# Kernel tuning notes

Hardware: AMD Instinct MI355X
Metric: run time of the kernel (lower is better)

## Reference

```python
import jax, jax.numpy as jnp
import numpy as np

N_NODES = 20000
HEADS = 4


def _gat_conv(x, src, dst, W, att_src, att_dst, bias, concat):
    # PyG GATConv: h = x @ W -> [N, H, C]; edge score = leaky_relu(a_s[src]+a_d[dst], 0.2);
    # segment softmax over dst; scatter-add weighted messages.
    N = x.shape[0]
    H, C = att_src.shape[1], att_src.shape[2]
    h = (x @ W).reshape(N, H, C)
    a_s = jnp.sum(h * att_src, axis=-1)  # [N, H]
    a_d = jnp.sum(h * att_dst, axis=-1)  # [N, H]
    e = jax.nn.leaky_relu(a_s[src] + a_d[dst], negative_slope=0.2)  # [E, H]
    m = jax.ops.segment_max(e, dst, num_segments=N)  # [N, H]
    e = jnp.exp(e - m[dst])
    denom = jax.ops.segment_sum(e, dst, num_segments=N)
    alpha = e / (denom[dst] + 1e-16)  # [E, H]
    msg = h[src] * alpha[:, :, None]  # [E, H, C]
    out = jax.ops.segment_sum(msg, dst, num_segments=N)  # [N, H, C]
    if concat:
        out = out.reshape(N, H * C)
    else:
        out = out.mean(axis=1)
    return out + bias


def setup_inputs() -> dict:
    key = jax.random.key(0)
    ks = jax.random.split(key, 16)
    N, F_in, Hd, H, Z = N_NODES, 256, 128, HEADS, 64
    E = 320000
    x = jax.random.normal(ks[0], (N, F_in), dtype=jnp.float32)
    edge_index = jax.random.randint(ks[1], (2, E), 0, N, dtype=jnp.int64)
    def xavier(k, shape):
        fan_in, fan_out = shape[0], shape[1]
        lim = float(np.sqrt(6.0 / (fan_in + fan_out)))
        return jax.random.uniform(k, shape, jnp.float32, -lim, lim)
    inp = {"x": x, "edge_index": edge_index}
    dims = [(F_in, Hd), (Hd * H, Hd), (Hd * H, Hd)]
    for i, (din, dout) in enumerate(dims, 1):
        inp[f"W{i}"] = xavier(ks[2 * i], (din, H * dout))
        inp[f"att{i}_src"] = jax.random.normal(ks[2 * i + 1], (1, H, dout), dtype=jnp.float32) * 0.1
        inp[f"att{i}_dst"] = jax.random.normal(jax.random.fold_in(ks[2 * i + 1], 7), (1, H, dout), dtype=jnp.float32) * 0.1
        bdim = H * dout if i < 3 else dout
        inp[f"b{i}"] = jnp.zeros((bdim,), dtype=jnp.float32)
    inp["fc_W"] = xavier(ks[10], (Hd, 2 * Z))
    inp["fc_b"] = jnp.zeros((2 * Z,), dtype=jnp.float32)
    return inp


def reference(x, edge_index, W1, att1_src, att1_dst, b1, W2, att2_src, att2_dst, b2,
              W3, att3_src, att3_dst, b3, fc_W, fc_b):
    N = x.shape[0]
    # add_self_loops=True (PyG default)
    loop = jnp.arange(N, dtype=edge_index.dtype)
    src = jnp.concatenate([edge_index[0], loop])
    dst = jnp.concatenate([edge_index[1], loop])
    h = jax.nn.leaky_relu(_gat_conv(x, src, dst, W1, att1_src, att1_dst, b1, True), 0.01)
    h = jax.nn.leaky_relu(_gat_conv(h, src, dst, W2, att2_src, att2_dst, b2, True), 0.01)
    h = _gat_conv(h, src, dst, W3, att3_src, att3_dst, b3, False)
    z = h @ fc_W + fc_b
    mu, logvar = jnp.split(z, 2, axis=1)
    return (mu, jnp.exp(logvar))
```

## Files before the change

### kernel.cpp

```cpp
#include <hip/hip_runtime.h>
#include <hip/hip_bf16.h>

typedef unsigned short u16;
typedef unsigned int u32;
typedef __attribute__((ext_vector_type(8))) short bf16x8;
typedef __attribute__((ext_vector_type(4))) float f32x4;
typedef __attribute__((ext_vector_type(8))) u16 u16x8;
typedef __attribute__((ext_vector_type(4))) u16 u16x4;

#define NN 20000
#define NE 320000
#define HC 512

__device__ __forceinline__ float bf2f(u16 u){ return __uint_as_float(((u32)u)<<16); }
__device__ __forceinline__ u16 f2bf(float x){
  __hip_bfloat16 h = __float2bfloat16(x);
  return *reinterpret_cast<u16*>(&h);
}
__device__ __forceinline__ float escore(float x){
  float e = x > 0.f ? x : 0.2f*x;
  return __expf(fminf(e, 80.f));
}

__global__ __launch_bounds__(256) void cast_kernel(const float* __restrict__ in, u16* __restrict__ out, int total){
  int i = (blockIdx.x*256 + threadIdx.x)*4;
  if (i >= total) return;
  float4 v = *(const float4*)(in + i);
  u16x4 o = { f2bf(v.x), f2bf(v.y), f2bf(v.z), f2bf(v.w) };
  *(u16x4*)(out + i) = o;
}

__global__ __launch_bounds__(256) void transpose_cast(const float* __restrict__ W, u16* __restrict__ WT,
                                                      int K, int N){
  __shared__ u16 t[32][33];
  int bx = blockIdx.x*32;
  int by = blockIdx.y*32;
  int tx = threadIdx.x & 31, ty = threadIdx.x >> 5;
  for (int r = ty; r < 32; r += 8) t[r][tx] = f2bf(W[(size_t)(by+r)*N + bx + tx]);
  __syncthreads();
  for (int r = ty; r < 32; r += 8) WT[(size_t)(bx+r)*K + by + tx] = t[tx][r];
}

__global__ void detect_kernel(const int* __restrict__ ei, int* __restrict__ flag){
  __shared__ int nz;
  if (threadIdx.x == 0) nz = 0;
  __syncthreads();
  int c = 0;
  for (int k = threadIdx.x; k < 4096; k += 256) if (ei[2*k + 1] != 0) c++;
  atomicAdd(&nz, c);
  __syncthreads();
  if (threadIdx.x == 0) *flag = (nz == 0) ? 1 : 0;
}

__global__ __launch_bounds__(256) void normalize_edges(const int* __restrict__ ei, const int* __restrict__ flag,
    int* __restrict__ src, int* __restrict__ dst, int E){
  int e = blockIdx.x*256 + threadIdx.x;
  if (e >= E) return;
  if (*flag){ src[e] = ei[2*e]; dst[e] = ei[2*(E + e)]; }
  else      { src[e] = ei[e];   dst[e] = ei[E + e]; }
}

__global__ __launch_bounds__(256) void gemm_bf16(const u16* __restrict__ A, const u16* __restrict__ BT,
                                                 u16* __restrict__ C, int M, int K){
  __shared__ __align__(16) u16 Ads[128][64];
  __shared__ __align__(16) u16 Bds[128][64];
  const int bm = blockIdx.x, bn = blockIdx.y;
  const int tid = threadIdx.x;
  const int lane = tid & 63, wid = tid >> 6;
  const int wr = (wid >> 1) << 6, wc = (wid & 1) << 6;
  f32x4 acc[4][4] = {};
  const int row0 = bm*128;
  for (int k0 = 0; k0 < K; k0 += 64){
    #pragma unroll
    for (int p = 0; p < 4; ++p){
      int idx = p*256 + tid;
      int r = idx >> 3;
      int c = (idx & 7) << 3;
      int cs = c ^ ((r & 7) << 3);
      u16x8 va = {};
      int gr = row0 + r;
      if (gr < M) va = *(const u16x8*)(A + (size_t)gr*K + k0 + c);
      *(u16x8*)&Ads[r][cs] = va;
      u16x8 vb = *(const u16x8*)(BT + (size_t)(bn*128 + r)*K + k0 + c);
      *(u16x8*)&Bds[r][cs] = vb;
    }
    __syncthreads();
    #pragma unroll
    for (int kk = 0; kk < 64; kk += 32){
      const int lr = lane & 15;
      const int lk = kk + ((lane >> 4) << 3);
      bf16x8 a[4], b[4];
      #pragma unroll
      for (int i = 0; i < 4; ++i){
        int ar = wr + 16*i + lr;
        a[i] = *(const bf16x8*)&Ads[ar][lk ^ ((ar & 7) << 3)];
      }
      #pragma unroll
      for (int j = 0; j < 4; ++j){
        int br = wc + 16*j + lr;
        b[j] = *(const bf16x8*)&Bds[br][lk ^ ((br & 7) << 3)];
      }
      #pragma unroll
      for (int i = 0; i < 4; ++i)
        #pragma unroll
        for (int j = 0; j < 4; ++j)
          acc[i][j] = __builtin_amdgcn_mfma_f32_16x16x32_bf16(a[i], b[j], acc[i][j], 0, 0, 0);
    }
    __syncthreads();
  }
  const int lr = lane & 15, r4 = (lane >> 4) << 2;
  #pragma unroll
  for (int i = 0; i < 4; ++i)
    #pragma unroll
    for (int j = 0; j < 4; ++j){
      int col = bn*128 + wc + 16*j + lr;
      #pragma unroll
      for (int r = 0; r < 4; ++r){
        int row = row0 + wr + 16*i + r4 + r;
        if (row < M) C[(size_t)row*HC + col] = f2bf(acc[i][j][r]);
      }
    }
}

__global__ __launch_bounds__(256) void asad_kernel(const u16* __restrict__ h,
    const float* __restrict__ attS, const float* __restrict__ attD,
    float* __restrict__ a_s, float* __restrict__ a_d, int N){
  int wid = blockIdx.x*4 + (threadIdx.x >> 6);
  if (wid >= N) return;
  int lane = threadIdx.x & 63;
  u16x8 v = *(const u16x8*)(h + (size_t)wid*HC + lane*8);
  float4 s0 = *(const float4*)(attS + lane*8);
  float4 s1 = *(const float4*)(attS + lane*8 + 4);
  float4 d0 = *(const float4*)(attD + lane*8);
  float4 d1 = *(const float4*)(attD + lane*8 + 4);
  float sv[8] = {s0.x,s0.y,s0.z,s0.w,s1.x,s1.y,s1.z,s1.w};
  float dv[8] = {d0.x,d0.y,d0.z,d0.w,d1.x,d1.y,d1.z,d1.w};
  float ps = 0.f, pd = 0.f;
  #pragma unroll
  for (int t = 0; t < 8; ++t){ float hv = bf2f(v[t]); ps += hv*sv[t]; pd += hv*dv[t]; }
  #pragma unroll
  for (int off = 1; off < 16; off <<= 1){
    ps += __shfl_xor(ps, off, 64);
    pd += __shfl_xor(pd, off, 64);
  }
  if ((lane & 15) == 0){
    int hh = lane >> 4;
    a_s[wid*4 + hh] = ps;
    a_d[wid*4 + hh] = pd;
  }
}

__global__ __launch_bounds__(256) void hist_kernel(const int* __restrict__ dst, int* __restrict__ cnt, int E){
  int e = blockIdx.x*256 + threadIdx.x;
  if (e < E) atomicAdd(&cnt[dst[e]], 1);
}

__global__ __launch_bounds__(1024) void scan_kernel(const int* __restrict__ cnt,
    int* __restrict__ offs, int* __restrict__ cur, int N){
  __shared__ int bsum[1024];
  int tid = threadIdx.x;
  const int CH = (N + 1023) >> 10;
  int lo = tid*CH, hi = min(lo + CH, N);
  int s = 0;
  for (int i = lo; i < hi; ++i) s += cnt[i];
  bsum[tid] = s;
  __syncthreads();
  for (int off = 1; off < 1024; off <<= 1){
    int t = (tid >= off) ? bsum[tid - off] : 0;
    __syncthreads();
    bsum[tid] += t;
    __syncthreads();
  }
  int run = (tid > 0) ? bsum[tid - 1] : 0;
  for (int i = lo; i < hi; ++i){
    offs[i] = run; cur[i] = run; run += cnt[i];
  }
  if (tid == 1023) offs[N] = bsum[1023];
}

__global__ __launch_bounds__(256) void scatter_kernel(const int* __restrict__ src, const int* __restrict__ dst,
    int* __restrict__ cur, int* __restrict__ src_sorted, int E){
  int e = blockIdx.x*256 + threadIdx.x;
  if (e >= E) return;
  int d = dst[e];
  int pos = atomicAdd(&cur[d], 1);
  src_sorted[pos] = src[e];
}

template<int MODE>
__global__ __launch_bounds__(256) void agg_kernel(const u16* __restrict__ h,
    const int* __restrict__ srcs, const int* __restrict__ offs,
    const float* __restrict__ a_s, const float* __restrict__ a_d,
    const float* __restrict__ bias, void* __restrict__ outp, int N){
  int d = blockIdx.x*4 + (threadIdx.x >> 6);
  if (d >= N) return;
  int lane = threadIdx.x & 63;
  int head = lane >> 4;
  float adv = a_d[d*4 + head];
  float acc[8];
  float dsum;
  {
    float w = escore(a_s[d*4 + head] + adv);
    dsum = w;
    u16x8 v = *(const u16x8*)(h + (size_t)d*HC + lane*8);
    #pragma unroll
    for (int t = 0; t < 8; ++t) acc[t] = w*bf2f(v[t]);
  }
  int p0 = offs[d], p1 = offs[d+1];
  int p = p0;
  for (; p + 3 < p1; p += 4){
    int s0 = srcs[p], s1 = srcs[p+1], s2 = srcs[p+2], s3 = srcs[p+3];
    float w0 = escore(a_s[s0*4 + head] + adv);
    float w1 = escore(a_s[s1*4 + head] + adv);
    float w2 = escore(a_s[s2*4 + head] + adv);
    float w3 = escore(a_s[s3*4 + head] + adv);
    u16x8 v0 = *(const u16x8*)(h + (size_t)s0*HC + lane*8);
    u16x8 v1 = *(const u16x8*)(h + (size_t)s1*HC + lane*8);
    u16x8 v2 = *(const u16x8*)(h + (size_t)s2*HC + lane*8);
    u16x8 v3 = *(const u16x8*)(h + (size_t)s3*HC + lane*8);
    dsum += w0 + w1 + w2 + w3;
    #pragma unroll
    for (int t = 0; t < 8; ++t)
      acc[t] += w0*bf2f(v0[t]) + w1*bf2f(v1[t]) + w2*bf2f(v2[t]) + w3*bf2f(v3[t]);
  }
  for (; p < p1; ++p){
    int s = srcs[p];
    float w = escore(a_s[s*4 + head] + adv);
    u16x8 v = *(const u16x8*)(h + (size_t)s*HC + lane*8);
    dsum += w;
    #pragma unroll
    for (int t = 0; t < 8; ++t) acc[t] += w*bf2f(v[t]);
  }
  float inv = 1.0f / (dsum + 1e-16f);
  if (MODE < 2){
    u16* act = (u16*)outp;
    u16x8 o;
    #pragma unroll
    for (int t = 0; t < 8; ++t){
      float x = acc[t]*inv + bias[lane*8 + t];
      x = x > 0.f ? x : 0.01f*x;
      o[t] = f2bf(x);
    }
    *(u16x8*)(act + (size_t)d*HC + lane*8) = o;
  } else {
    #pragma unroll
    for (int t = 0; t < 8; ++t){
      acc[t] *= inv;
      acc[t] += __shfl_xor(acc[t], 16, 64);
      acc[t] += __shfl_xor(acc[t], 32, 64);
    }
    if (lane < 16){
      float* hf = (float*)outp;
      int c0 = lane*8;
      float4 o0 = {0.25f*acc[0] + bias[c0+0], 0.25f*acc[1] + bias[c0+1],
                   0.25f*acc[2] + bias[c0+2], 0.25f*acc[3] + bias[c0+3]};
      float4 o1 = {0.25f*acc[4] + bias[c0+4], 0.25f*acc[5] + bias[c0+5],
                   0.25f*acc[6] + bias[c0+6], 0.25f*acc[7] + bias[c0+7]};
      *(float4*)(hf + (size_t)d*128 + c0)     = o0;
      *(float4*)(hf + (size_t)d*128 + c0 + 4) = o1;
    }
  }
}

__global__ __launch_bounds__(128) void fc_kernel(const float* __restrict__ hfin, const float* __restrict__ W,
    const float* __restrict__ b, float* __restrict__ outp, int N){
  __shared__ float hl[128];
  int n = blockIdx.x, o = threadIdx.x;
  hl[o] = hfin[(size_t)n*128 + o];
  __syncthreads();
  float acc = b[o];
  #pragma unroll 8
  for (int k = 0; k < 128; ++k) acc += hl[k]*W[k*128 + o];
  if (o < 64) outp[(size_t)n*64 + o] = acc;
  else        outp[(size_t)N*64 + (size_t)n*64 + (o - 64)] = expf(acc);
}

extern "C" void kernel_launch(void* const* d_in, const int* in_sizes, int n_in,
                              void* d_out, int out_size, void* d_ws, size_t ws_size,
                              hipStream_t stream){
  const float* x    = (const float*)d_in[0];
  const int* ei     = (const int*)d_in[1];
  const float* W1   = (const float*)d_in[2];
  const float* att1s= (const float*)d_in[3];
  const float* att1d= (const float*)d_in[4];
  const float* b1   = (const float*)d_in[5];
  const float* W2   = (const float*)d_in[6];
  const float* att2s= (const float*)d_in[7];
  const float* att2d= (const float*)d_in[8];
  const float* b2   = (const float*)d_in[9];
  const float* W3   = (const float*)d_in[10];
  const float* att3s= (const float*)d_in[11];
  const float* att3d= (const float*)d_in[12];
  const float* b3   = (const float*)d_in[13];
  const float* fcW  = (const float*)d_in[14];
  const float* fcb  = (const float*)d_in[15];
  float* outp = (float*)d_out;

  char* ws = (char*)d_ws;
  size_t off = 0;
  auto alloc = [&](size_t bytes) -> void* {
    void* p = ws + off;
    off = (off + bytes + 255) & ~(size_t)255;
    return p;
  };
  u16*   xb     = (u16*)  alloc((size_t)NN*256*2);
  u16*   h      = (u16*)  alloc((size_t)NN*HC*2);
  u16*   act    = (u16*)  alloc((size_t)NN*HC*2);
  float* hfin   = (float*)alloc((size_t)NN*128*4);
  float* a_s    = (float*)alloc((size_t)NN*4*4);
  float* a_d    = (float*)alloc((size_t)NN*4*4);
  int*   cnt    = (int*)  alloc((size_t)NN*4);
  int*   cur    = (int*)  alloc((size_t)NN*4);
  int*   offs   = (int*)  alloc((size_t)(NN+1)*4);
  int*   src32  = (int*)  alloc((size_t)NE*4);
  int*   dst32  = (int*)  alloc((size_t)NE*4);
  int*   srcs   = (int*)  alloc((size_t)NE*4);
  u16*   WT1    = (u16*)  alloc((size_t)512*256*2);
  u16*   WT2    = (u16*)  alloc((size_t)512*512*2);
  u16*   WT3    = (u16*)  alloc((size_t)512*512*2);
  int*   flag   = (int*)  alloc(256);

  cast_kernel<<<5000, 256, 0, stream>>>(x, xb, NN*256);
  transpose_cast<<<dim3(16, 8),  256, 0, stream>>>(W1, WT1, 256, 512);
  transpose_cast<<<dim3(16, 16), 256, 0, stream>>>(W2, WT2, 512, 512);
  transpose_cast<<<dim3(16, 16), 256, 0, stream>>>(W3, WT3, 512, 512);

  detect_kernel<<<1, 256, 0, stream>>>(ei, flag);
  normalize_edges<<<1250, 256, 0, stream>>>(ei, flag, src32, dst32, NE);

  hipMemsetAsync(cnt, 0, (size_t)NN*4, stream);
  hist_kernel<<<1250, 256, 0, stream>>>(dst32, cnt, NE);
  scan_kernel<<<1, 1024, 0, stream>>>(cnt, offs, cur, NN);
  scatter_kernel<<<1250, 256, 0, stream>>>(src32, dst32, cur, srcs, NE);

  const float* attS[3] = {att1s, att2s, att3s};
  const float* attD[3] = {att1d, att2d, att3d};
  const u16*   WT[3]   = {WT1, WT2, WT3};
  const int    Kd[3]   = {256, 512, 512};

  for (int layer = 0; layer < 3; ++layer){
    const u16* Ain = (layer == 0) ? xb : act;
    gemm_bf16<<<dim3(157, 4), 256, 0, stream>>>(Ain, WT[layer], h, NN, Kd[layer]);
    asad_kernel<<<5000, 256, 0, stream>>>(h, attS[layer], attD[layer], a_s, a_d, NN);
    if (layer == 0)
      agg_kernel<0><<<5000, 256, 0, stream>>>(h, srcs, offs, a_s, a_d, b1, act, NN);
    else if (layer == 1)
      agg_kernel<1><<<5000, 256, 0, stream>>>(h, srcs, offs, a_s, a_d, b2, act, NN);
    else
      agg_kernel<2><<<5000, 256, 0, stream>>>(h, srcs, offs, a_s, a_d, b3, hfin, NN);
  }

  fc_kernel<<<NN, 128, 0, stream>>>(hfin, fcW, fcb, outp, NN);
}
```

Before: 351.2 us.

## Move final FC to split-bf16 MFMA GEMM and use direct global-to-LDS loads

Replaces the scalar per-node FC kernel with an MFMA GEMM that splits fp32 activations and weights into bf16 hi/lo parts and runs three products to keep near-fp32 accuracy. It also switches the main GEMM tile loads to global_load_lds so data goes straight into swizzled shared memory without passing through registers. The aim is to cut the FC cost, which previously reread the whole weight matrix for every node, and to reduce load overhead in the GEMM. In exchange it adds split kernels, extra buffers and launches, and depends on the lane-to-LDS layout of the direct loads matching the XOR swizzle.

```diff
diff --git a/kernel.cpp b/kernel.cpp
--- a/kernel.cpp
+++ b/kernel.cpp
@@ -20,6 +20,12 @@
 __device__ __forceinline__ float escore(float x){
   float e = x > 0.f ? x : 0.2f*x;
   return __expf(fminf(e, 80.f));
+}
+
+typedef const __attribute__((address_space(1))) unsigned int* gas_t;
+typedef __attribute__((address_space(3))) unsigned int* las_t;
+__device__ __forceinline__ void gl16(const void* g, void* l){
+  __builtin_amdgcn_global_load_lds((gas_t)g, (las_t)l, 16, 0, 0);
 }
 
 __global__ __launch_bounds__(256) void cast_kernel(const float* __restrict__ in, u16* __restrict__ out, int total){
@@ -70,19 +76,16 @@
   const int wr = (wid >> 1) << 6, wc = (wid & 1) << 6;
   f32x4 acc[4][4] = {};
   const int row0 = bm*128;
+  const int wbase = tid & 192;
   for (int k0 = 0; k0 < K; k0 += 64){
     #pragma unroll
     for (int p = 0; p < 4; ++p){
       int idx = p*256 + tid;
-      int r = idx >> 3;
-      int c = (idx & 7) << 3;
-      int cs = c ^ ((r & 7) << 3);
-      u16x8 va = {};
-      int gr = row0 + r;
-      if (gr < M) va = *(const u16x8*)(A + (size_t)gr*K + k0 + c);
-      *(u16x8*)&Ads[r][cs] = va;
-      u16x8 vb = *(const u16x8*)(BT + (size_t)(bn*128 + r)*K + k0 + c);
-      *(u16x8*)&Bds[r][cs] = vb;
+      int r = idx >> 3, cg = idx & 7;
+      int csg = cg ^ (r & 7);
+      int gr = row0 + r; if (gr >= M) gr = M - 1;
+      gl16(A + (size_t)gr*K + k0 + csg*8, (u16*)Ads + (size_t)(p*256 + wbase)*8);
+      gl16(BT + (size_t)(bn*128 + r)*K + k0 + csg*8, (u16*)Bds + (size_t)(p*256 + wbase)*8);
     }
     __syncthreads();
     #pragma unroll
@@ -262,17 +265,106 @@
   }
 }
 
-__global__ __launch_bounds__(128) void fc_kernel(const float* __restrict__ hfin, const float* __restrict__ W,
-    const float* __restrict__ b, float* __restrict__ outp, int N){
-  __shared__ float hl[128];
-  int n = blockIdx.x, o = threadIdx.x;
-  hl[o] = hfin[(size_t)n*128 + o];
-  __syncthreads();
-  float acc = b[o];
-  #pragma unroll 8
-  for (int k = 0; k < 128; ++k) acc += hl[k]*W[k*128 + o];
-  if (o < 64) outp[(size_t)n*64 + o] = acc;
-  else        outp[(size_t)N*64 + (size_t)n*64 + (o - 64)] = expf(acc);
+__global__ __launch_bounds__(256) void hsplit_kernel(const float* __restrict__ hfin,
+    u16* __restrict__ Hhi, u16* __restrict__ Hlo, int total){
+  int i = (blockIdx.x*256 + threadIdx.x)*4;
+  if (i >= total) return;
+  float4 v = *(const float4*)(hfin + i);
+  float r[4] = {v.x, v.y, v.z, v.w};
+  u16x4 hi, lo;
+  #pragma unroll
+  for (int t = 0; t < 4; ++t){
+    hi[t] = f2bf(r[t]);
+    lo[t] = f2bf(r[t] - bf2f(hi[t]));
+  }
+  *(u16x4*)(Hhi + i) = hi;
+  *(u16x4*)(Hlo + i) = lo;
+}
+
+__global__ __launch_bounds__(256) void wsplit_kernel(const float* __restrict__ W,
+    u16* __restrict__ WThi, u16* __restrict__ WTlo){
+  int i = blockIdx.x*256 + threadIdx.x;
+  int k = i >> 7, o = i & 127;
+  float w = W[i];
+  u16 hi = f2bf(w);
+  u16 lo = f2bf(w - bf2f(hi));
+  WThi[o*128 + k] = hi;
+  WTlo[o*128 + k] = lo;
+}
+
+__global__ __launch_bounds__(256) void fc_mfma(const u16* __restrict__ Hhi, const u16* __restrict__ Hlo,
+    const u16* __restrict__ WThi, const u16* __restrict__ WTlo,
+    const float* __restrict__ fcb, float* __restrict__ outp, int M){
+  __shared__ __align__(16) u16 Ahi[128][64];
+  __shared__ __align__(16) u16 Alo[128][64];
+  __shared__ __align__(16) u16 Bhi[128][64];
+  __shared__ __align__(16) u16 Blo[128][64];
+  const int tid = threadIdx.x;
+  const int lane = tid & 63, wid = tid >> 6;
+  const int wr = (wid >> 1) << 6, wc = (wid & 1) << 6;
+  f32x4 acc[4][4] = {};
+  const int row0 = blockIdx.x*128;
+  for (int k0 = 0; k0 < 128; k0 += 64){
+    #pragma unroll
+    for (int p = 0; p < 4; ++p){
+      int idx = p*256 + tid;
+      int r = idx >> 3;
+      int c = (idx & 7) << 3;
+      int cs = c ^ ((r & 7) << 3);
+      int gr = row0 + r; if (gr >= M) gr = M - 1;
+      *(u16x8*)&Ahi[r][cs] = *(const u16x8*)(Hhi + (size_t)gr*128 + k0 + c);
+      *(u16x8*)&Alo[r][cs] = *(const u16x8*)(Hlo + (size_t)gr*128 + k0 + c);
+      *(u16x8*)&Bhi[r][cs] = *(const u16x8*)(WThi + (size_t)r*128 + k0 + c);
+      *(u16x8*)&Blo[r][cs] = *(const u16x8*)(WTlo + (size_t)r*128 + k0 + c);
+    }
+    __syncthreads();
+    #pragma unroll
+    for (int kk = 0; kk < 64; kk += 32){
+      const int lr = lane & 15;
+      const int lk = kk + ((lane >> 4) << 3);
+      bf16x8 ah[4], al[4], bh[4], bl[4];
+      #pragma unroll
+      for (int i = 0; i < 4; ++i){
+        int ar = wr + 16*i + lr;
+        int sw = lk ^ ((ar & 7) << 3);
+        ah[i] = *(const bf16x8*)&Ahi[ar][sw];
+        al[i] = *(const bf16x8*)&Alo[ar][sw];
+      }
+      #pragma unroll
+      for (int j = 0; j < 4; ++j){
+        int br = wc + 16*j + lr;
+        int sw = lk ^ ((br & 7) << 3);
+        bh[j] = *(const bf16x8*)&Bhi[br][sw];
+        bl[j] = *(const bf16x8*)&Blo[br][sw];
+      }
+      #pragma unroll
+      for (int i = 0; i < 4; ++i)
+        #pragma unroll
+        for (int j = 0; j < 4; ++j){
+          acc[i][j] = __builtin_amdgcn_mfma_f32_16x16x32_bf16(ah[i], bh[j], acc[i][j], 0, 0, 0);
+          acc[i][j] = __builtin_amdgcn_mfma_f32_16x16x32_bf16(ah[i], bl[j], acc[i][j], 0, 0, 0);
+          acc[i][j] = __builtin_amdgcn_mfma_f32_16x16x32_bf16(al[i], bh[j], acc[i][j], 0, 0, 0);
+        }
+    }
+    __syncthreads();
+  }
+  const int lr = lane & 15, r4 = (lane >> 4) << 2;
+  #pragma unroll
+  for (int i = 0; i < 4; ++i)
+    #pragma unroll
+    for (int j = 0; j < 4; ++j){
+      int o = wc + 16*j + lr;
+      float bb = fcb[o];
+      #pragma unroll
+      for (int r = 0; r < 4; ++r){
+        int row = row0 + wr + 16*i + r4 + r;
+        if (row < M){
+          float z = acc[i][j][r] + bb;
+          if (o < 64) outp[(size_t)row*64 + o] = z;
+          else        outp[(size_t)M*64 + (size_t)row*64 + (o - 64)] = expf(z);
+        }
+      }
+    }
 }
 
 extern "C" void kernel_launch(void* const* d_in, const int* in_sizes, int n_in,
@@ -307,6 +399,8 @@
   u16*   h      = (u16*)  alloc((size_t)NN*HC*2);
   u16*   act    = (u16*)  alloc((size_t)NN*HC*2);
   float* hfin   = (float*)alloc((size_t)NN*128*4);
+  u16*   Hhi    = (u16*)  alloc((size_t)NN*128*2);
+  u16*   Hlo    = (u16*)  alloc((size_t)NN*128*2);
   float* a_s    = (float*)alloc((size_t)NN*4*4);
   float* a_d    = (float*)alloc((size_t)NN*4*4);
   int*   cnt    = (int*)  alloc((size_t)NN*4);
@@ -318,12 +412,15 @@
   u16*   WT1    = (u16*)  alloc((size_t)512*256*2);
   u16*   WT2    = (u16*)  alloc((size_t)512*512*2);
   u16*   WT3    = (u16*)  alloc((size_t)512*512*2);
+  u16*   WThi   = (u16*)  alloc((size_t)128*128*2);
+  u16*   WTlo   = (u16*)  alloc((size_t)128*128*2);
   int*   flag   = (int*)  alloc(256);
 
   cast_kernel<<<5000, 256, 0, stream>>>(x, xb, NN*256);
   transpose_cast<<<dim3(16, 8),  256, 0, stream>>>(W1, WT1, 256, 512);
   transpose_cast<<<dim3(16, 16), 256, 0, stream>>>(W2, WT2, 512, 512);
   transpose_cast<<<dim3(16, 16), 256, 0, stream>>>(W3, WT3, 512, 512);
+  wsplit_kernel<<<64, 256, 0, stream>>>(fcW, WThi, WTlo);
 
   detect_kernel<<<1, 256, 0, stream>>>(ei, flag);
   normalize_edges<<<1250, 256, 0, stream>>>(ei, flag, src32, dst32, NE);
@@ -350,5 +447,6 @@
       agg_kernel<2><<<5000, 256, 0, stream>>>(h, srcs, offs, a_s, a_d, b3, hfin, NN);
   }
 
-  fc_kernel<<<NN, 128, 0, stream>>>(hfin, fcW, fcb, outp, NN);
-}
+  hsplit_kernel<<<2500, 256, 0, stream>>>(hfin, Hhi, Hlo, NN*128);
+  fc_mfma<<<157, 256, 0, stream>>>(Hhi, Hlo, WThi, WTlo, fcb, outp, NN);
+}
```

New measurement: 325.9 us. 7.2% less time.
